# Performance work log

Hardware: AMD Instinct MI355X
Metric: run time of the kernel (lower is better)

The kernel has to match this reference:

```python
import jax, jax.numpy as jnp
import numpy as np

B, C, H, W = 8, 128, 64, 64
KC = 32  # key_channels

def setup_inputs() -> dict:
    key = jax.random.key(0)
    ks = jax.random.split(key, 6)
    s = lambda fan_in: 1.0 / np.sqrt(fan_in)
    x  = jax.random.normal(ks[0], (B, C, H, W), dtype=jnp.float32)
    Wq = jax.random.uniform(ks[1], (KC, C), jnp.float32, -s(C), s(C))  # 1x1 conv kernels
    Wk = jax.random.uniform(ks[2], (KC, C), jnp.float32, -s(C), s(C))
    Wv = jax.random.uniform(ks[3], (C, C), jnp.float32, -s(C), s(C))
    Wo = jax.random.uniform(ks[4], (C, C), jnp.float32, -s(C), s(C))
    gamma = jnp.zeros((1,), jnp.float32) + 0.1  # nonzero so attention path matters
    return {"x": x, "Wq": Wq, "Wk": Wk, "Wv": Wv, "Wo": Wo, "gamma": gamma}

def reference(x, Wq, Wk, Wv, Wo, gamma):
    b, c, h, w = x.shape
    xf = x.reshape(b, c, h * w)                      # [B,C,N]
    Q = jnp.einsum('qc,bcn->bnq', Wq, xf)            # [B,N,KC]
    K = jnp.einsum('kc,bcn->bkn', Wk, xf)            # [B,KC,N]
    V = jnp.einsum('vc,bcn->bnv', Wv, xf)            # [B,N,C]
    scores = jnp.einsum('bnq,bqm->bnm', Q, K) / jnp.sqrt(jnp.asarray(Wq.shape[0], x.dtype))
    attn = jax.nn.softmax(scores, axis=-1)           # [B,N,N]
    out = jnp.einsum('bnm,bmv->bvn', attn, V)        # [B,C,N]
    out = jnp.einsum('oc,bcn->bon', Wo, out).reshape(b, c, h, w)
    return x + gamma * out
```

## Files before the change

### kernel.cpp

```cpp
#include <hip/hip_runtime.h>
#include <hip/hip_bf16.h>

#define BB 8
#define CC 128
#define NN 4096
#define KCQ 32

typedef unsigned short u16;
typedef unsigned int u32;
typedef unsigned char u8;
typedef __bf16 bf16x8 __attribute__((ext_vector_type(8)));
typedef float f32x4 __attribute__((ext_vector_type(4)));
typedef long i64;
typedef long i64x2 __attribute__((ext_vector_type(2)));

typedef const __attribute__((address_space(1))) void gas_t;
typedef __attribute__((address_space(3))) void las_t;

__device__ __forceinline__ u16 f2bf(float f){
  u32 u = __builtin_bit_cast(u32, f);
  u32 r = u + 0x7FFFu + ((u >> 16) & 1u);
  return (u16)(r >> 16);
}
__device__ __forceinline__ u32 cvtpk(float lo, float hi){
  u32 r; asm("v_cvt_pk_bf16_f32 %0, %1, %2" : "=v"(r) : "v"(lo), "v"(hi)); return r;
}
__device__ __forceinline__ u32 pk_fp8x4(float a, float b, float c, float d){
  int v = 0;
  v = __builtin_amdgcn_cvt_pk_fp8_f32(a, b, v, false);
  v = __builtin_amdgcn_cvt_pk_fp8_f32(c, d, v, true);
  return (u32)v;
}
__device__ __forceinline__ void gload16(const void* g, void* l){
  __builtin_amdgcn_global_load_lds((gas_t*)g, (las_t*)l, 16, 0, 0);
}

__global__ __launch_bounds__(256) void k_prep_w(const float* Wq, const float* Wk,
                                                const float* Wv, const float* Wo,
                                                u16* wsq, u16* wsk, u16* wsv, u16* wso){
  int i = blockIdx.x * 256 + threadIdx.x;
  const float SC = 0.2550350f;
  if (i < 4096)       wsq[i]        = f2bf(Wq[i] * SC);
  else if (i < 8192)  wsk[i-4096]   = f2bf(Wk[i-4096]);
  else if (i < 24576) wsv[i-8192]   = f2bf(Wv[i-8192]);
  else if (i < 40960) wso[i-24576]  = f2bf(Wo[i-24576]);
}

__global__ __launch_bounds__(512) void k_projx(const float* x, const u16* wq, const u16* wk,
                                               const u16* wv, u16* Qm, u16* Km, u8* Vt8){
  __shared__ __align__(16) u16 xL[64*132];
  __shared__ __align__(16) u16 wvL[128*132];
  int b = blockIdx.x >> 6, nb = (blockIdx.x & 63) * 64;
  int t = threadIdx.x;
  int n = t & 63, cg = t >> 6;
  #pragma unroll
  for (int it = 0; it < 16; ++it){
    int c = it*8 + cg;
    xL[n*132 + c] = f2bf(x[((size_t)b*CC + c)*NN + nb + n]);
  }
  {
    int r = t >> 2, c0 = (t & 3) * 32;
    const u32* src = (const u32*)wv + r*64 + (t&3)*16;
    #pragma unroll
    for (int j = 0; j < 16; ++j)
      *(u32*)(wvL + r*132 + c0 + j*2) = src[j];
  }
  __syncthreads();
  int w = t >> 6, l = t & 63, a = l & 15, g = l >> 4;
  int ns = w >> 1, half = w & 1;
  int n0 = nb + ns*16;
  bf16x8 xa[4];
  #pragma unroll
  for (int kc = 0; kc < 4; ++kc)
    xa[kc] = *(const bf16x8*)(xL + (ns*16 + a)*132 + kc*32 + g*8);
  __syncthreads();

  u32* vbuf = (u32*)xL;
  auto Vjob = [&](int vt){
    f32x4 acc = {0.f,0.f,0.f,0.f};
    #pragma unroll
    for (int kc = 0; kc < 4; ++kc){
      bf16x8 wa = *(const bf16x8*)(wvL + (vt*16 + a)*132 + kc*32 + g*8);
      acc = __builtin_amdgcn_mfma_f32_16x16x32_bf16(xa[kc], wa, acc, 0,0,0);
    }
    int row = vt*16 + a;
    vbuf[row*16 + ((ns ^ ((a>>1)&3)) << 2) + g] = pk_fp8x4(acc[0], acc[1], acc[2], acc[3]);
  };

  if (half == 0){
    #pragma unroll
    for (int qt = 0; qt < 2; ++qt){
      f32x4 accq = {0.f,0.f,0.f,0.f}, acck = {0.f,0.f,0.f,0.f};
      #pragma unroll
      for (int kc = 0; kc < 4; ++kc){
        bf16x8 wbq = ((const bf16x8*)(wq + (size_t)(qt*16 + a) * CC))[kc*4 + g];
        bf16x8 wbk = ((const bf16x8*)(wk + (size_t)(qt*16 + a) * CC))[kc*4 + g];
        accq = __builtin_amdgcn_mfma_f32_16x16x32_bf16(xa[kc], wbq, accq, 0,0,0);
        acck = __builtin_amdgcn_mfma_f32_16x16x32_bf16(xa[kc], wbk, acck, 0,0,0);
      }
      #pragma unroll
      for (int r = 0; r < 4; ++r){
        Qm[((size_t)b*NN + n0 + 4*g + r) * KCQ + qt*16 + a] = f2bf(accq[r]);
        Km[((size_t)b*NN + n0 + 4*g + r) * KCQ + qt*16 + a] = f2bf(acck[r]);
      }
    }
    Vjob(0); Vjob(1);
  } else {
    #pragma unroll
    for (int vt = 2; vt < 8; ++vt) Vjob(vt);
  }
  __syncthreads();
  {
    int row = t >> 2, gg = t & 3, key = (row >> 1) & 3;
    const u32* vb = vbuf + row*16;
    auto rd = [&](int d){ return vb[(((d>>2)^key)<<2) + (d&3)]; };
    uint4 dd;
    dd.x = rd(2*gg);     dd.y = rd(2*gg+1);
    dd.z = rd(8+2*gg);   dd.w = rd(9+2*gg);
    *(uint4*)(Vt8 + ((size_t)b*CC + row)*NN + nb + gg*16) = dd;
  }
}

__global__ __launch_bounds__(512, 4) void k_attn(const u16* Qm, const u16* Km,
                                                 const u8* Vt8, const u16* wso,
                                                 const float* x, const float* gamma,
                                                 float* out){
  __shared__ __align__(16) char smem[49152];
  int bid = blockIdx.x;
  int b = bid & 7, qb = bid >> 3;
  int t0 = threadIdx.x;
  int l = t0 & 63, a = l & 15, g = l >> 4;
  int w = t0 >> 6;
  int q0 = qb * 64;

  const u8* Vb = Vt8 + (size_t)b * CC * NN;

  bf16x8 qf[4];
  #pragma unroll
  for (int qs = 0; qs < 4; ++qs)
    qf[qs] = ((const bf16x8*)(Qm + ((size_t)b*NN + q0 + qs*16 + a) * KCQ))[g];
  const u16* kPtr = Km + ((size_t)b*NN + w*16 + a) * KCQ + g*8;

  f32x4 o[4];
  #pragma unroll
  for (int i = 0; i < 4; ++i) o[i] = (f32x4){0.f,0.f,0.f,0.f};
  float ls[4] = {0.f, 0.f, 0.f, 0.f};

  int srcCh = ((l&7) ^ ((l>>3)&7)) << 4;
  const u8* vS0 = Vb + (size_t)(w*16 + (l>>3))*NN + srcCh;
  const u8* vS1 = vS0 + (size_t)8*NN;
  const int vOff = w*2048 + l*16;
  auto stageV = [&](int kt, int sl){
    char* bs = smem + (sl << 14);
    gload16(vS0 + kt*128, bs + vOff);
    gload16(vS1 + kt*128, bs + vOff + 1024);
  };

  const int Cg = ((w>>2)<<2) | ((w&1)<<1) | (g>>1);
  const int ppos = ((Cg ^ (a&7)) << 4) | (((w>>1)&1) << 3) | ((g&1) << 2);
  auto SM = [&](const f32x4* sv, char* Pw){
    #pragma unroll
    for (int qs = 0; qs < 4; ++qs){
      float p0 = __builtin_amdgcn_exp2f(sv[qs][0]);
      float p1 = __builtin_amdgcn_exp2f(sv[qs][1]);
      float p2 = __builtin_amdgcn_exp2f(sv[qs][2]);
      float p3 = __builtin_amdgcn_exp2f(sv[qs][3]);
      ls[qs] += (p0 + p1) + (p2 + p3);
      *(u32*)(Pw + (qs*16 + a)*128 + ppos) = pk_fp8x4(p0, p1, p2, p3);
    }
  };

  const int rc0 = (g ^ (a&7)) << 4;
  const int rc1 = ((4 + g) ^ (a&7)) << 4;
  auto PV = [&](int sl){
    const char* Vs = smem + (sl << 14);
    const char* Pr = smem + 32768 + (sl << 13);
    __builtin_amdgcn_s_setprio(1);
    i64x2 vf0 = *(const i64x2*)(Vs + (w*16 + a)*128 + rc0);
    i64x2 vf1 = *(const i64x2*)(Vs + (w*16 + a)*128 + rc1);
    #pragma unroll
    for (int qs = 0; qs < 4; ++qs){
      i64x2 pf0 = *(const i64x2*)(Pr + (qs*16 + a)*128 + rc0);
      i64x2 pf1 = *(const i64x2*)(Pr + (qs*16 + a)*128 + rc1);
      o[qs] = __builtin_amdgcn_mfma_f32_16x16x32_fp8_fp8(vf0[0], pf0[0], o[qs], 0,0,0);
      o[qs] = __builtin_amdgcn_mfma_f32_16x16x32_fp8_fp8(vf0[1], pf0[1], o[qs], 0,0,0);
      o[qs] = __builtin_amdgcn_mfma_f32_16x16x32_fp8_fp8(vf1[0], pf1[0], o[qs], 0,0,0);
      o[qs] = __builtin_amdgcn_mfma_f32_16x16x32_fp8_fp8(vf1[1], pf1[1], o[qs], 0,0,0);
    }
    __builtin_amdgcn_s_setprio(0);
  };

  stageV(0, 0);
  bf16x8 kfB = *(const bf16x8*)kPtr;
  bf16x8 kfA = *(const bf16x8*)(kPtr + 4096);
  {
    f32x4 sv[4];
    #pragma unroll
    for (int qs = 0; qs < 4; ++qs){
      f32x4 z = {0.f,0.f,0.f,0.f};
      sv[qs] = __builtin_amdgcn_mfma_f32_16x16x32_bf16(kfB, qf[qs], z, 0,0,0);
    }
    SM(sv, smem + 32768);
  }
  asm volatile("s_waitcnt vmcnt(0) lgkmcnt(0)" ::: "memory");
  __builtin_amdgcn_s_barrier();
  kfB = kfA;

  for (int t = 0; t < 31; ++t){
    stageV(t+1, (t+1)&1);
    f32x4 sv[4];
    #pragma unroll
    for (int qs = 0; qs < 4; ++qs){
      f32x4 z = {0.f,0.f,0.f,0.f};
      sv[qs] = __builtin_amdgcn_mfma_f32_16x16x32_bf16(kfB, qf[qs], z, 0,0,0);
    }
    PV(t & 1);
    SM(sv, smem + 32768 + (((t+1)&1) << 13));
    if (t < 30){
      kfA = *(const bf16x8*)(kPtr + (size_t)(t+2)*4096);
      asm volatile("s_waitcnt vmcnt(1) lgkmcnt(0)" ::: "memory");
    } else {
      asm volatile("s_waitcnt vmcnt(0) lgkmcnt(0)" ::: "memory");
    }
    __builtin_amdgcn_s_barrier();
    kfB = kfA;
  }
  PV(1);

  #pragma unroll
  for (int qs = 0; qs < 4; ++qs){
    ls[qs] += __shfl_xor(ls[qs], 16);
    ls[qs] += __shfl_xor(ls[qs], 32);
  }
  __syncthreads();
  float* Ml = (float*)smem;
  if (l < 16){
    #pragma unroll
    for (int qs = 0; qs < 4; ++qs) Ml[w*64 + qs*16 + l] = ls[qs];
  }
  __syncthreads();
  u16* Ol = (u16*)(smem + 4096);
  #pragma unroll
  for (int qs = 0; qs < 4; ++qs){
    float lsum = 0.f;
    #pragma unroll
    for (int ww = 0; ww < 8; ++ww) lsum += Ml[ww*64 + qs*16 + a];
    float inv = 1.f / lsum;
    f32x4 oc = o[qs];
    uint2 pk;
    pk.x = cvtpk(oc[0]*inv, oc[1]*inv);
    pk.y = cvtpk(oc[2]*inv, oc[3]*inv);
    int chunk = (w*2 + (g>>1)) ^ (a & 7);
    *(uint2*)((char*)Ol + (qs*16 + a)*256 + chunk*16 + (g&1)*8) = pk;
  }
  __syncthreads();
  float gm = gamma[0];
  f32x4 acc2[4];
  #pragma unroll
  for (int qs = 0; qs < 4; ++qs) acc2[qs] = (f32x4){0.f,0.f,0.f,0.f};
  #pragma unroll
  for (int kc = 0; kc < 4; ++kc){
    bf16x8 wof = *(const bf16x8*)(wso + (size_t)(w*16 + a)*CC + kc*32 + g*8);
    #pragma unroll
    for (int qs = 0; qs < 4; ++qs){
      int chunk = (kc*4 + g) ^ (a & 7);
      bf16x8 of = *(const bf16x8*)((const char*)Ol + (qs*16 + a)*256 + chunk*16);
      acc2[qs] = __builtin_amdgcn_mfma_f32_16x16x32_bf16(wof, of, acc2[qs], 0,0,0);
    }
  }
  #pragma unroll
  for (int qs = 0; qs < 4; ++qs){
    #pragma unroll
    for (int r = 0; r < 4; ++r){
      size_t idx = ((size_t)b*CC + w*16 + 4*g + r)*NN + q0 + qs*16 + a;
      out[idx] = x[idx] + gm * acc2[qs][r];
    }
  }
}

extern "C" void kernel_launch(void* const* d_in, const int* in_sizes, int n_in,
                              void* d_out, int out_size, void* d_ws, size_t ws_size,
                              hipStream_t stream) {
  const float* x     = (const float*)d_in[0];
  const float* Wq    = (const float*)d_in[1];
  const float* Wk    = (const float*)d_in[2];
  const float* Wv    = (const float*)d_in[3];
  const float* Wo    = (const float*)d_in[4];
  const float* gamma = (const float*)d_in[5];
  float* out = (float*)d_out;

  u16* wsq = (u16*)d_ws;
  u16* wsk = wsq + 4096;
  u16* wsv = wsk + 4096;
  u16* wso = wsv + 16384;
  u16* Qm  = wso + 16384;
  u16* Km  = Qm + (size_t)BB*NN*KCQ;
  u8*  Vt8 = (u8*)(Km + (size_t)BB*NN*KCQ);

  hipLaunchKernelGGL(k_prep_w, dim3(160), dim3(256), 0, stream, Wq, Wk, Wv, Wo, wsq, wsk, wsv, wso);
  hipLaunchKernelGGL(k_projx,  dim3(512), dim3(512), 0, stream, x, wsq, wsk, wsv, Qm, Km, Vt8);
  hipLaunchKernelGGL(k_attn,   dim3(512), dim3(512), 0, stream, Qm, Km, Vt8, wso, x, gamma, out);
}
```

Before: 64.16 us.

## Fuse weight conversion into kernels and triple-buffer V staging in attention

Removes the separate weight-preparation kernel; projection and attention kernels now read fp32 weights and convert to bf16 inline with the packed convert instruction. The attention kernel's V tiles move from double to triple buffering, with stage issue placed after the softmax so loads run further ahead, and LDS grows to 64KB. This removes a launch and an intermediate buffer, but adds redundant per-block weight conversion and higher LDS use that may reduce resident blocks per CU.

```diff
diff --git a/kernel.cpp b/kernel.cpp
--- a/kernel.cpp
+++ b/kernel.cpp
@@ -17,11 +17,6 @@
 typedef const __attribute__((address_space(1))) void gas_t;
 typedef __attribute__((address_space(3))) void las_t;
 
-__device__ __forceinline__ u16 f2bf(float f){
-  u32 u = __builtin_bit_cast(u32, f);
-  u32 r = u + 0x7FFFu + ((u >> 16) & 1u);
-  return (u16)(r >> 16);
-}
 __device__ __forceinline__ u32 cvtpk(float lo, float hi){
   u32 r; asm("v_cvt_pk_bf16_f32 %0, %1, %2" : "=v"(r) : "v"(lo), "v"(hi)); return r;
 }
@@ -34,20 +29,19 @@
 __device__ __forceinline__ void gload16(const void* g, void* l){
   __builtin_amdgcn_global_load_lds((gas_t*)g, (las_t*)l, 16, 0, 0);
 }
-
-__global__ __launch_bounds__(256) void k_prep_w(const float* Wq, const float* Wk,
-                                                const float* Wv, const float* Wo,
-                                                u16* wsq, u16* wsk, u16* wsv, u16* wso){
-  int i = blockIdx.x * 256 + threadIdx.x;
-  const float SC = 0.2550350f;
-  if (i < 4096)       wsq[i]        = f2bf(Wq[i] * SC);
-  else if (i < 8192)  wsk[i-4096]   = f2bf(Wk[i-4096]);
-  else if (i < 24576) wsv[i-8192]   = f2bf(Wv[i-8192]);
-  else if (i < 40960) wso[i-24576]  = f2bf(Wo[i-24576]);
-}
-
-__global__ __launch_bounds__(512) void k_projx(const float* x, const u16* wq, const u16* wk,
-                                               const u16* wv, u16* Qm, u16* Km, u8* Vt8){
+__device__ __forceinline__ bf16x8 ldw8(const float* p, float sc){
+  f32x4 v0 = *(const f32x4*)p, v1 = *(const f32x4*)(p + 4);
+  uint4 u;
+  u.x = cvtpk(v0[0]*sc, v0[1]*sc);
+  u.y = cvtpk(v0[2]*sc, v0[3]*sc);
+  u.z = cvtpk(v1[0]*sc, v1[1]*sc);
+  u.w = cvtpk(v1[2]*sc, v1[3]*sc);
+  return __builtin_bit_cast(bf16x8, u);
+}
+
+__global__ __launch_bounds__(512) void k_projx(const float* x, const float* Wq,
+                                               const float* Wk, const float* Wv,
+                                               u16* Qm, u16* Km, u8* Vt8){
   __shared__ __align__(16) u16 xL[64*132];
   __shared__ __align__(16) u16 wvL[128*132];
   int b = blockIdx.x >> 6, nb = (blockIdx.x & 63) * 64;
@@ -56,14 +50,18 @@
   #pragma unroll
   for (int it = 0; it < 16; ++it){
     int c = it*8 + cg;
-    xL[n*132 + c] = f2bf(x[((size_t)b*CC + c)*NN + nb + n]);
+    u32 pk = cvtpk(x[((size_t)b*CC + c)*NN + nb + n], 0.f);
+    xL[n*132 + c] = (u16)pk;
   }
   {
     int r = t >> 2, c0 = (t & 3) * 32;
-    const u32* src = (const u32*)wv + r*64 + (t&3)*16;
-    #pragma unroll
-    for (int j = 0; j < 16; ++j)
-      *(u32*)(wvL + r*132 + c0 + j*2) = src[j];
+    const float* src = Wv + (size_t)r*CC + c0;
+    #pragma unroll
+    for (int j = 0; j < 8; ++j){
+      f32x4 v = *(const f32x4*)(src + j*4);
+      *(u32*)(wvL + r*132 + c0 + j*4)     = cvtpk(v[0], v[1]);
+      *(u32*)(wvL + r*132 + c0 + j*4 + 2) = cvtpk(v[2], v[3]);
+    }
   }
   __syncthreads();
   int w = t >> 6, l = t & 63, a = l & 15, g = l >> 4;
@@ -87,21 +85,22 @@
     vbuf[row*16 + ((ns ^ ((a>>1)&3)) << 2) + g] = pk_fp8x4(acc[0], acc[1], acc[2], acc[3]);
   };
 
+  const float SC = 0.2550350f;
   if (half == 0){
     #pragma unroll
     for (int qt = 0; qt < 2; ++qt){
       f32x4 accq = {0.f,0.f,0.f,0.f}, acck = {0.f,0.f,0.f,0.f};
       #pragma unroll
       for (int kc = 0; kc < 4; ++kc){
-        bf16x8 wbq = ((const bf16x8*)(wq + (size_t)(qt*16 + a) * CC))[kc*4 + g];
-        bf16x8 wbk = ((const bf16x8*)(wk + (size_t)(qt*16 + a) * CC))[kc*4 + g];
+        bf16x8 wbq = ldw8(Wq + (size_t)(qt*16 + a)*CC + kc*32 + g*8, SC);
+        bf16x8 wbk = ldw8(Wk + (size_t)(qt*16 + a)*CC + kc*32 + g*8, 1.0f);
         accq = __builtin_amdgcn_mfma_f32_16x16x32_bf16(xa[kc], wbq, accq, 0,0,0);
         acck = __builtin_amdgcn_mfma_f32_16x16x32_bf16(xa[kc], wbk, acck, 0,0,0);
       }
       #pragma unroll
       for (int r = 0; r < 4; ++r){
-        Qm[((size_t)b*NN + n0 + 4*g + r) * KCQ + qt*16 + a] = f2bf(accq[r]);
-        Km[((size_t)b*NN + n0 + 4*g + r) * KCQ + qt*16 + a] = f2bf(acck[r]);
+        Qm[((size_t)b*NN + n0 + 4*g + r) * KCQ + qt*16 + a] = (u16)cvtpk(accq[r], 0.f);
+        Km[((size_t)b*NN + n0 + 4*g + r) * KCQ + qt*16 + a] = (u16)cvtpk(acck[r], 0.f);
       }
     }
     Vjob(0); Vjob(1);
@@ -122,10 +121,10 @@
 }
 
 __global__ __launch_bounds__(512, 4) void k_attn(const u16* Qm, const u16* Km,
-                                                 const u8* Vt8, const u16* wso,
+                                                 const u8* Vt8, const float* Wo,
                                                  const float* x, const float* gamma,
                                                  float* out){
-  __shared__ __align__(16) char smem[49152];
+  __shared__ __align__(16) char smem[65536];
   int bid = blockIdx.x;
   int b = bid & 7, qb = bid >> 3;
   int t0 = threadIdx.x;
@@ -152,8 +151,8 @@
   const int vOff = w*2048 + l*16;
   auto stageV = [&](int kt, int sl){
     char* bs = smem + (sl << 14);
-    gload16(vS0 + kt*128, bs + vOff);
-    gload16(vS1 + kt*128, bs + vOff + 1024);
+    gload16(vS0 + (size_t)kt*128, bs + vOff);
+    gload16(vS1 + (size_t)kt*128, bs + vOff + 1024);
   };
 
   const int Cg = ((w>>2)<<2) | ((w&1)<<1) | (g>>1);
@@ -172,9 +171,9 @@
 
   const int rc0 = (g ^ (a&7)) << 4;
   const int rc1 = ((4 + g) ^ (a&7)) << 4;
-  auto PV = [&](int sl){
-    const char* Vs = smem + (sl << 14);
-    const char* Pr = smem + 32768 + (sl << 13);
+  auto PV = [&](int ps, int vsl){
+    const char* Vs = smem + (vsl << 14);
+    const char* Pr = smem + 49152 + (ps << 13);
     __builtin_amdgcn_s_setprio(1);
     i64x2 vf0 = *(const i64x2*)(Vs + (w*16 + a)*128 + rc0);
     i64x2 vf1 = *(const i64x2*)(Vs + (w*16 + a)*128 + rc1);
@@ -190,42 +189,46 @@
     __builtin_amdgcn_s_setprio(0);
   };
 
+  bf16x8 kfC = *(const bf16x8*)kPtr;
+  bf16x8 kfN = *(const bf16x8*)(kPtr + 4096);
   stageV(0, 0);
-  bf16x8 kfB = *(const bf16x8*)kPtr;
-  bf16x8 kfA = *(const bf16x8*)(kPtr + 4096);
+  stageV(1, 1);
   {
     f32x4 sv[4];
     #pragma unroll
     for (int qs = 0; qs < 4; ++qs){
       f32x4 z = {0.f,0.f,0.f,0.f};
-      sv[qs] = __builtin_amdgcn_mfma_f32_16x16x32_bf16(kfB, qf[qs], z, 0,0,0);
-    }
-    SM(sv, smem + 32768);
-  }
-  asm volatile("s_waitcnt vmcnt(0) lgkmcnt(0)" ::: "memory");
+      sv[qs] = __builtin_amdgcn_mfma_f32_16x16x32_bf16(kfC, qf[qs], z, 0,0,0);
+    }
+    SM(sv, smem + 49152);
+  }
+  asm volatile("s_waitcnt vmcnt(2) lgkmcnt(0)" ::: "memory");
   __builtin_amdgcn_s_barrier();
-  kfB = kfA;
-
+  kfC = kfN;
+
+  int vR = 0;
   for (int t = 0; t < 31; ++t){
-    stageV(t+1, (t+1)&1);
     f32x4 sv[4];
     #pragma unroll
     for (int qs = 0; qs < 4; ++qs){
       f32x4 z = {0.f,0.f,0.f,0.f};
-      sv[qs] = __builtin_amdgcn_mfma_f32_16x16x32_bf16(kfB, qf[qs], z, 0,0,0);
-    }
-    PV(t & 1);
-    SM(sv, smem + 32768 + (((t+1)&1) << 13));
+      sv[qs] = __builtin_amdgcn_mfma_f32_16x16x32_bf16(kfC, qf[qs], z, 0,0,0);
+    }
+    PV(t & 1, vR);
+    SM(sv, smem + 49152 + (((t+1)&1) << 13));
     if (t < 30){
-      kfA = *(const bf16x8*)(kPtr + (size_t)(t+2)*4096);
-      asm volatile("s_waitcnt vmcnt(1) lgkmcnt(0)" ::: "memory");
+      kfN = *(const bf16x8*)(kPtr + (size_t)(t+2)*4096);
+      int sl = vR >= 1 ? vR - 1 : 2;
+      stageV(t+2, sl);
+      asm volatile("s_waitcnt vmcnt(3) lgkmcnt(0)" ::: "memory");
     } else {
       asm volatile("s_waitcnt vmcnt(0) lgkmcnt(0)" ::: "memory");
     }
     __builtin_amdgcn_s_barrier();
-    kfB = kfA;
-  }
-  PV(1);
+    kfC = kfN;
+    vR = (vR == 2) ? 0 : vR + 1;
+  }
+  PV(1, vR);
 
   #pragma unroll
   for (int qs = 0; qs < 4; ++qs){
@@ -260,7 +263,7 @@
   for (int qs = 0; qs < 4; ++qs) acc2[qs] = (f32x4){0.f,0.f,0.f,0.f};
   #pragma unroll
   for (int kc = 0; kc < 4; ++kc){
-    bf16x8 wof = *(const bf16x8*)(wso + (size_t)(w*16 + a)*CC + kc*32 + g*8);
+    bf16x8 wof = ldw8(Wo + (size_t)(w*16 + a)*CC + kc*32 + g*8, 1.0f);
     #pragma unroll
     for (int qs = 0; qs < 4; ++qs){
       int chunk = (kc*4 + g) ^ (a & 7);
@@ -289,15 +292,10 @@
   const float* gamma = (const float*)d_in[5];
   float* out = (float*)d_out;
 
-  u16* wsq = (u16*)d_ws;
-  u16* wsk = wsq + 4096;
-  u16* wsv = wsk + 4096;
-  u16* wso = wsv + 16384;
-  u16* Qm  = wso + 16384;
+  u16* Qm  = (u16*)d_ws;
   u16* Km  = Qm + (size_t)BB*NN*KCQ;
   u8*  Vt8 = (u8*)(Km + (size_t)BB*NN*KCQ);
 
-  hipLaunchKernelGGL(k_prep_w, dim3(160), dim3(256), 0, stream, Wq, Wk, Wv, Wo, wsq, wsk, wsv, wso);
-  hipLaunchKernelGGL(k_projx,  dim3(512), dim3(512), 0, stream, x, wsq, wsk, wsv, Qm, Km, Vt8);
-  hipLaunchKernelGGL(k_attn,   dim3(512), dim3(512), 0, stream, Qm, Km, Vt8, wso, x, gamma, out);
-}
+  hipLaunchKernelGGL(k_projx, dim3(512), dim3(512), 0, stream, x, Wq, Wk, Wv, Qm, Km, Vt8);
+  hipLaunchKernelGGL(k_attn,  dim3(512), dim3(512), 0, stream, Qm, Km, Vt8, Wo, x, gamma, out);
+}
```

After: 65.10 us. No clear change (+1.5%).
